# Kernel optimization log

Measured on AMD Instinct MI355X. Metric: run time of the kernel, lower is better.

Reference implementation:

```python
import jax, jax.numpy as jnp
import numpy as np

NUM_REL = 8
NUM_NODE = 100000
TYPED_NUM_NODE = 50000   # typed_num_node per relation (static)
EDGES_PER_REL = 800000   # avg degree 16
IN_C = 128
HID_C = 128


def setup_inputs() -> dict:
    key = jax.random.key(0)
    k1, k2, k3, k4, k5 = jax.random.split(key, 5)
    x = jax.random.normal(k1, (NUM_NODE, IN_C), dtype=jnp.float32)
    rel_weight = jax.random.normal(k2, (NUM_REL, IN_C, HID_C), dtype=jnp.float32) * 0.05
    sub_ptr = jnp.sort(jax.random.randint(k3, (NUM_REL, TYPED_NUM_NODE + 1), 0, EDGES_PER_REL), axis=-1)
    sub_idx = jax.random.randint(k4, (NUM_REL, EDGES_PER_REL), 0, NUM_NODE)
    sub_target = jax.random.randint(k5, (NUM_REL, TYPED_NUM_NODE), 0, NUM_NODE)
    return {"x": x, "rel_weight": rel_weight, "sub_ptr": sub_ptr,
            "sub_idx": sub_idx, "sub_target": sub_target}


def _csr_segment_ids(ptr):
    # CSR ptr [N+1] -> per-edge destination segment id [E]
    e = jnp.arange(EDGES_PER_REL)
    return jnp.clip(jnp.searchsorted(ptr, e, side='right') - 1, 0, TYPED_NUM_NODE - 1)


def reference(x, rel_weight, sub_ptr, sub_idx, sub_target):
    outs = []
    for r in range(NUM_REL):  # small fixed relation count
        seg = _csr_segment_ids(sub_ptr[r])
        # sage_sum_forward: sum neighbor features per destination node
        agg = jax.ops.segment_sum(x[sub_idx[r]], seg, num_segments=TYPED_NUM_NODE)  # [T, C]
        outs.append(agg @ rel_weight[r])  # [T, H]
    arr = jnp.concatenate(outs, axis=0)            # [R*T, H]
    tgt = sub_target.reshape(-1)                   # [R*T]
    out = jnp.zeros((NUM_NODE, HID_C), dtype=x.dtype).at[tgt].add(arr)
    return out
```

## Files before the change

kernel.cpp:

```cpp
#include <hip/hip_runtime.h>

#define NREL 8
#define NNODE 100000
#define TNODE 50000
#define NEDGE 800000
#define C 128
#define TILE_T 64
#define NTILE ((TNODE + TILE_T - 1) / TILE_T)
#define NENT (NREL * TNODE)
#define NB_SCAN ((NNODE + 255) / 256)

typedef unsigned int u32;
typedef unsigned short u16;
typedef __attribute__((ext_vector_type(8))) short bf16x8;
typedef __attribute__((ext_vector_type(4))) float f32x4;
typedef __attribute__((ext_vector_type(2))) float f32x2;

__device__ __forceinline__ u16 f2bf(float f) {
    union { float f; u32 u; } c; c.f = f;
    u32 u = c.u + 0x7FFFu + ((c.u >> 16) & 1u);
    return (u16)(u >> 16);
}
__device__ __forceinline__ u32 pack2(float a, float b) {
    return (u32)f2bf(a) | ((u32)f2bf(b) << 16);
}
__device__ __forceinline__ float2 unpack_bf2(u32 p) {
    union { u32 u; float f; } a, b;
    a.u = p << 16; b.u = p & 0xFFFF0000u;
    return make_float2(a.f, b.f);
}
__device__ __forceinline__ f32x2 bits2(u32 p) {
    union { u32 u[2]; f32x2 f; } c;
    c.u[0] = p << 16; c.u[1] = p & 0xFFFF0000u;
    return c.f;
}
__device__ __forceinline__ void addp(f32x2* a, uint4 v) {
    a[0] += bits2(v.x); a[1] += bits2(v.y);
    a[2] += bits2(v.z); a[3] += bits2(v.w);
}
__device__ __forceinline__ void fma4(float4& acc, float a, float w0, float w1, float w2, float w3) {
    acc.x = fmaf(a, w0, acc.x);
    acc.y = fmaf(a, w1, acc.y);
    acc.z = fmaf(a, w2, acc.z);
    acc.w = fmaf(a, w3, acc.w);
}

__global__ __launch_bounds__(256)
void convert_x_kernel(const float* __restrict__ x, u16* __restrict__ xb, int n4) {
    int i = blockIdx.x * 256 + threadIdx.x;
    const int stride = gridDim.x * 256;
    for (; i < n4; i += stride) {
        const float4 v = ((const float4*)x)[i];
        ushort4 o;
        o.x = f2bf(v.x); o.y = f2bf(v.y); o.z = f2bf(v.z); o.w = f2bf(v.w);
        ((ushort4*)xb)[i] = o;
    }
}

__global__ __launch_bounds__(256)
void convert_w_kernel(const float* __restrict__ w, u16* __restrict__ wtb) {
    const int o = blockIdx.x * 256 + threadIdx.x;
    if (o < NREL * C * C) {
        const int r = o >> 14, rem = o & 16383, cc = rem >> 7, k = rem & 127;
        wtb[o] = f2bf(w[(r << 14) + k * C + cc]);
    }
}

__global__ __launch_bounds__(256)
void hist_kernel(const int* __restrict__ tgt, int* __restrict__ count) {
    const int g = blockIdx.x * 256 + threadIdx.x;
    if (g < NENT) atomicAdd(&count[tgt[g]], 1);
}

__global__ __launch_bounds__(256)
void scan1_kernel(const int* __restrict__ count, int* __restrict__ bsum,
                  int* __restrict__ offsets, int* __restrict__ cursor) {
    __shared__ int s[256];
    const int tid = threadIdx.x;
    const int i = blockIdx.x * 256 + tid;
    const int v = (i < NNODE) ? count[i] : 0;
    s[tid] = v;
    __syncthreads();
    for (int st = 1; st < 256; st <<= 1) {
        const int t = (tid >= st) ? s[tid - st] : 0;
        __syncthreads();
        s[tid] += t;
        __syncthreads();
    }
    if (i < NNODE) {
        const int loc = s[tid] - v;
        offsets[i] = loc;
        cursor[i]  = loc;
    }
    if (tid == 255) bsum[blockIdx.x] = s[255];
}

__global__ __launch_bounds__(512)
void scan2_kernel(int* __restrict__ bsum) {
    __shared__ int s[512];
    const int tid = threadIdx.x;
    const int v = (tid < NB_SCAN) ? bsum[tid] : 0;
    s[tid] = v;
    __syncthreads();
    for (int st = 1; st < 512; st <<= 1) {
        const int t = (tid >= st) ? s[tid - st] : 0;
        __syncthreads();
        s[tid] += t;
        __syncthreads();
    }
    if (tid < NB_SCAN) bsum[tid] = s[tid] - v;
}

__global__ __launch_bounds__(256)
void fill_kernel(const int* __restrict__ tgt, int* __restrict__ cursor,
                 const int* __restrict__ bsum, int* __restrict__ list) {
    const int g = blockIdx.x * 256 + threadIdx.x;
    if (g < NENT) {
        const int t = tgt[g];
        const int pos = atomicAdd(&cursor[t], 1) + bsum[t >> 8];
        list[pos] = g;
    }
}

__global__ __launch_bounds__(512, 8)
void fused_gather_gemm_kernel(const u16* __restrict__ xb, const int* __restrict__ ptr,
                              const int* __restrict__ idx, const u16* __restrict__ wtb,
                              u16* __restrict__ P) {
    __shared__ u16 sA[TILE_T * 136];
    __shared__ int qcount;

    const int tid  = threadIdx.x;
    const int tile = blockIdx.x;
    const int r    = blockIdx.y;
    const int w    = tid >> 6;
    const int lane = tid & 63;

    if (tid == 0) qcount = 0;
    __syncthreads();

    const int* pr = ptr + r * (TNODE + 1);
    const int* er = idx + (size_t)r * NEDGE;
    const int q  = lane >> 4;
    const int sl = lane & 15;
    const u16* xcol = xb + sl * 8;

    for (;;) {
        int tl;
        if (lane == 0) tl = atomicAdd(&qcount, 1);
        tl = __shfl(tl, 0);
        if (tl >= TILE_T) break;

        const int t = tile * TILE_T + tl;
        f32x2 accA[4], accB[4];
        #pragma unroll
        for (int j = 0; j < 4; ++j) { accA[j] = (f32x2){0.f, 0.f}; accB[j] = (f32x2){0.f, 0.f}; }

        if (t < TNODE) {
            const int start = (t == 0) ? 0 : pr[t];
            const int end   = (t == TNODE - 1) ? NEDGE : pr[t + 1];

            for (int base = start; base < end; base += 64) {
                const int cnt = min(end - base, 64);
                int myi = (lane < cnt) ? er[base + lane] : 0;
                int i = 0;
                for (; i + 8 <= cnt; i += 8) {
                    const int sA0 = __shfl(myi, i + q);
                    const int sB0 = __shfl(myi, i + 4 + q);
                    const uint4 vA = *(const uint4*)(xcol + (size_t)sA0 * C);
                    const uint4 vB = *(const uint4*)(xcol + (size_t)sB0 * C);
                    addp(accA, vA);
                    addp(accB, vB);
                }
                if (i + 4 <= cnt) {
                    const int sA0 = __shfl(myi, i + q);
                    const uint4 vA = *(const uint4*)(xcol + (size_t)sA0 * C);
                    addp(accA, vA);
                    i += 4;
                }
                if (i < cnt) {
                    const int rem = cnt - i;
                    const int sA0 = __shfl(myi, i + ((q < rem) ? q : 0));
                    if (q < rem) {
                        const uint4 vA = *(const uint4*)(xcol + (size_t)sA0 * C);
                        addp(accA, vA);
                    }
                }
            }
        }
        #pragma unroll
        for (int j = 0; j < 4; ++j) {
            accA[j] += accB[j];
            accA[j].x += __shfl_xor(accA[j].x, 16);
            accA[j].y += __shfl_xor(accA[j].y, 16);
            accA[j].x += __shfl_xor(accA[j].x, 32);
            accA[j].y += __shfl_xor(accA[j].y, 32);
        }
        if (q == 0) {
            uint4 o;
            o.x = pack2(accA[0].x, accA[0].y);
            o.y = pack2(accA[1].x, accA[1].y);
            o.z = pack2(accA[2].x, accA[2].y);
            o.w = pack2(accA[3].x, accA[3].y);
            *(uint4*)(sA + tl * 136 + sl * 8) = o;
        }
    }
    __syncthreads();

    const int wr    = (w & 3) * 16;
    const int cbase = (w >> 2) * 4;
    const int fr    = lane & 15;
    const int fq    = lane >> 4;
    const u16* wb   = wtb + (size_t)r * C * C;

    f32x4 acc[4];
    #pragma unroll
    for (int cf = 0; cf < 4; ++cf) acc[cf] = (f32x4){0.f, 0.f, 0.f, 0.f};

    #pragma unroll
    for (int ks = 0; ks < 4; ++ks) {
        const bf16x8 a = *(const bf16x8*)(sA + (wr + fr) * 136 + ks * 32 + fq * 8);
        #pragma unroll
        for (int cf = 0; cf < 4; ++cf) {
            const bf16x8 b = *(const bf16x8*)(wb + ((cbase + cf) * 16 + fr) * C + ks * 32 + fq * 8);
            acc[cf] = __builtin_amdgcn_mfma_f32_16x16x32_bf16(a, b, acc[cf], 0, 0, 0);
        }
    }
    __syncthreads();

    #pragma unroll
    for (int cf = 0; cf < 4; ++cf) {
        #pragma unroll
        for (int j = 0; j < 4; ++j) {
            const int row = wr + fq * 4 + j;
            sA[row * 136 + (cbase + cf) * 16 + fr] = f2bf(acc[cf][j]);
        }
    }
    __syncthreads();

    #pragma unroll
    for (int i = 0; i < 2; ++i) {
        const int f = tid + i * 512;
        const int row = f >> 4, unit = f & 15;
        const int t = tile * TILE_T + row;
        if (t < TNODE)
            *(uint4*)(P + ((size_t)r * TNODE + t) * C + unit * 8) =
                *(const uint4*)(sA + row * 136 + unit * 8);
    }
}

__global__ __launch_bounds__(256)
void out_gather_kernel(const u16* __restrict__ P, const int* __restrict__ offsets,
                       const int* __restrict__ count, const int* __restrict__ bsum,
                       const int* __restrict__ list, float* __restrict__ out) {
    const int lane = threadIdx.x & 63;
    const int n = blockIdx.x * 4 + (threadIdx.x >> 6);
    if (n >= NNODE) return;
    const int st = offsets[n] + bsum[n >> 8];
    const int en = st + count[n];
    float2 a0 = make_float2(0.f, 0.f), a1 = make_float2(0.f, 0.f);
    int i = st;
    for (; i + 2 <= en; i += 2) {
        const u32 v0 = ((const u32*)(P + (size_t)list[i] * C))[lane];
        const u32 v1 = ((const u32*)(P + (size_t)list[i + 1] * C))[lane];
        const float2 f0 = unpack_bf2(v0), f1 = unpack_bf2(v1);
        a0.x += f0.x; a0.y += f0.y;
        a1.x += f1.x; a1.y += f1.y;
    }
    if (i < en) {
        const float2 f0 = unpack_bf2(((const u32*)(P + (size_t)list[i] * C))[lane]);
        a0.x += f0.x; a0.y += f0.y;
    }
    a0.x += a1.x; a0.y += a1.y;
    ((float2*)(out + (size_t)n * C))[lane] = a0;
}

__device__ __forceinline__ void add4(float4& acc, const float4& b) {
    acc.x += b.x; acc.y += b.y; acc.z += b.z; acc.w += b.w;
}
__global__ __launch_bounds__(256, 1)
void rgcn_fused_kernel(const float* __restrict__ x, const float* __restrict__ w,
                       const int* __restrict__ ptr, const int* __restrict__ idx,
                       const int* __restrict__ tgt, float* __restrict__ out) {
    __shared__ float sW[C * C];
    __shared__ float sAgg[TILE_T][C + 4];
    const int tid = threadIdx.x, tile = blockIdx.x, r = blockIdx.y;
    {
        const float4* src = (const float4*)(w + (size_t)r * C * C);
        float4* dst = (float4*)sW;
        #pragma unroll
        for (int i = 0; i < 16; ++i) dst[tid + i * 256] = src[tid + i * 256];
    }
    {
        const int tl = tid >> 2, g = tid & 3;
        const int t = tile * TILE_T + tl;
        float4 a[8];
        #pragma unroll
        for (int j = 0; j < 8; ++j) a[j] = make_float4(0.f, 0.f, 0.f, 0.f);
        if (t < TNODE) {
            const int* pr = ptr + (size_t)r * (TNODE + 1);
            const int* er = idx + (size_t)r * NEDGE;
            int e = (t == 0) ? 0 : pr[t];
            const int end = (t == TNODE - 1) ? NEDGE : pr[t + 1];
            for (; e < end; ++e) {
                const int s0 = er[e];
                const float4* r0 = (const float4*)(x + (size_t)s0 * C) + g * 8;
                #pragma unroll
                for (int j = 0; j < 8; ++j) add4(a[j], r0[j]);
            }
        }
        float* rowp = &sAgg[tl][g * 32];
        #pragma unroll
        for (int j = 0; j < 8; ++j) ((float4*)rowp)[j] = a[j];
    }
    __syncthreads();
    const int tg = tid >> 4, cg = tid & 15;
    float4 acc0[4], acc1[4];
    #pragma unroll
    for (int i = 0; i < 4; ++i) {
        acc0[i] = make_float4(0.f, 0.f, 0.f, 0.f);
        acc1[i] = make_float4(0.f, 0.f, 0.f, 0.f);
    }
    for (int k4 = 0; k4 < C / 4; ++k4) {
        float4 av[4];
        #pragma unroll
        for (int i = 0; i < 4; ++i) av[i] = *(const float4*)&sAgg[tg * 4 + i][k4 * 4];
        #pragma unroll
        for (int kk = 0; kk < 4; ++kk) {
            const int k = k4 * 4 + kk;
            const float4 w0 = *(const float4*)&sW[k * C + cg * 4];
            const float4 w1 = *(const float4*)&sW[k * C + 64 + cg * 4];
            #pragma unroll
            for (int i = 0; i < 4; ++i) {
                const float a = ((const float*)&av[i])[kk];
                fma4(acc0[i], a, w0.x, w0.y, w0.z, w0.w);
                fma4(acc1[i], a, w1.x, w1.y, w1.z, w1.w);
            }
        }
    }
    const int* tr = tgt + (size_t)r * TNODE;
    #pragma unroll
    for (int i = 0; i < 4; ++i) {
        const int t = tile * TILE_T + tg * 4 + i;
        if (t < TNODE) {
            const int node = tr[t];
            float* ob = out + (size_t)node * C + cg * 4;
            unsafeAtomicAdd(ob + 0, acc0[i].x);  unsafeAtomicAdd(ob + 1, acc0[i].y);
            unsafeAtomicAdd(ob + 2, acc0[i].z);  unsafeAtomicAdd(ob + 3, acc0[i].w);
            unsafeAtomicAdd(ob + 64, acc1[i].x); unsafeAtomicAdd(ob + 65, acc1[i].y);
            unsafeAtomicAdd(ob + 66, acc1[i].z); unsafeAtomicAdd(ob + 67, acc1[i].w);
        }
    }
}

extern "C" void kernel_launch(void* const* d_in, const int* in_sizes, int n_in,
                              void* d_out, int out_size, void* d_ws, size_t ws_size,
                              hipStream_t stream) {
    const float* x   = (const float*)d_in[0];
    const float* w   = (const float*)d_in[1];
    const int*   ptr = (const int*)d_in[2];
    const int*   idx = (const int*)d_in[3];
    const int*   tgt = (const int*)d_in[4];
    float* out = (float*)d_out;

    const size_t WS_NEED = 135000000;
    char* base = (char*)d_ws;

    if (ws_size >= WS_NEED) {
        u16* P       = (u16*)(base + 0);
        u16* xb      = (u16*)(base + 104000000);
        u16* wtb     = (u16*)(base + 130000000);
        int* count   = (int*)(base + 131000000);
        int* offsets = (int*)(base + 131500000);
        int* cursor  = (int*)(base + 132000000);
        int* bsum    = (int*)(base + 132500000);
        int* list    = (int*)(base + 133000000);

        convert_x_kernel<<<2048, 256, 0, stream>>>(x, xb, NNODE * C / 4);
        convert_w_kernel<<<(NREL * C * C + 255) / 256, 256, 0, stream>>>(w, wtb);

        hipMemsetAsync(count, 0, NNODE * sizeof(int), stream);
        hist_kernel<<<(NENT + 255) / 256, 256, 0, stream>>>(tgt, count);
        scan1_kernel<<<NB_SCAN, 256, 0, stream>>>(count, bsum, offsets, cursor);
        scan2_kernel<<<1, 512, 0, stream>>>(bsum);
        fill_kernel<<<(NENT + 255) / 256, 256, 0, stream>>>(tgt, cursor, bsum, list);

        dim3 grid(NTILE, NREL);
        fused_gather_gemm_kernel<<<grid, 512, 0, stream>>>(xb, ptr, idx, wtb, P);

        out_gather_kernel<<<(NNODE + 3) / 4, 256, 0, stream>>>(P, offsets, count, bsum, list, out);
    } else {
        hipMemsetAsync(out, 0, (size_t)NNODE * C * sizeof(float), stream);
        dim3 grid(NTILE, NREL);
        rgcn_fused_kernel<<<grid, 256, 0, stream>>>(x, w, ptr, idx, tgt, out);
    }
}
```

Measured before the change: 368.1 us.

## Fuse setup kernels and stage relation weights in LDS for MFMA

Combines the x conversion, weight transpose-conversion and count zeroing into a single launch, removing two kernel launches and a memset. In the fused gather-GEMM kernel, the per-relation bf16 weight matrix is first copied into a padded shared-memory buffer and the MFMA B operands are read from it instead of global memory. This adds about 34KB of LDS per block and lowers the occupancy hint from 8 to 6 blocks. Every tile now reloads the full 32KB weight matrix even though it reads each element once, so LDS pressure could cut occupancy during the gather phase.

```diff
diff --git a/kernel.cpp b/kernel.cpp
--- a/kernel.cpp
+++ b/kernel.cpp
@@ -10,6 +10,10 @@
 #define NENT (NREL * TNODE)
 #define NB_SCAN ((NNODE + 255) / 256)
 
+#define NB_CVX (NNODE * C / 4 / 256)
+#define NB_CVW (NREL * C * C / 256)
+#define NB_ZERO NB_SCAN
+
 typedef unsigned int u32;
 typedef unsigned short u16;
 typedef __attribute__((ext_vector_type(8))) short bf16x8;
@@ -46,23 +50,24 @@
 }
 
 __global__ __launch_bounds__(256)
-void convert_x_kernel(const float* __restrict__ x, u16* __restrict__ xb, int n4) {
-    int i = blockIdx.x * 256 + threadIdx.x;
-    const int stride = gridDim.x * 256;
-    for (; i < n4; i += stride) {
+void setup_kernel(const float* __restrict__ x, u16* __restrict__ xb,
+                  const float* __restrict__ w, u16* __restrict__ wtb,
+                  int* __restrict__ count) {
+    const int b = blockIdx.x;
+    const int tid = threadIdx.x;
+    if (b < NB_CVX) {
+        const int i = b * 256 + tid;
         const float4 v = ((const float4*)x)[i];
         ushort4 o;
         o.x = f2bf(v.x); o.y = f2bf(v.y); o.z = f2bf(v.z); o.w = f2bf(v.w);
         ((ushort4*)xb)[i] = o;
-    }
-}
-
-__global__ __launch_bounds__(256)
-void convert_w_kernel(const float* __restrict__ w, u16* __restrict__ wtb) {
-    const int o = blockIdx.x * 256 + threadIdx.x;
-    if (o < NREL * C * C) {
+    } else if (b < NB_CVX + NB_CVW) {
+        const int o = (b - NB_CVX) * 256 + tid;
         const int r = o >> 14, rem = o & 16383, cc = rem >> 7, k = rem & 127;
         wtb[o] = f2bf(w[(r << 14) + k * C + cc]);
+    } else {
+        const int i = (b - NB_CVX - NB_CVW) * 256 + tid;
+        if (i < NNODE) count[i] = 0;
     }
 }
 
@@ -122,10 +127,11 @@
     }
 }
 
-__global__ __launch_bounds__(512, 8)
+__global__ __launch_bounds__(512, 6)
 void fused_gather_gemm_kernel(const u16* __restrict__ xb, const int* __restrict__ ptr,
                               const int* __restrict__ idx, const u16* __restrict__ wtb,
                               u16* __restrict__ P) {
+    __shared__ u16 sB[C * 136];
     __shared__ u16 sA[TILE_T * 136];
     __shared__ int qcount;
 
@@ -135,6 +141,15 @@
     const int w    = tid >> 6;
     const int lane = tid & 63;
 
+    {
+        const uint4* src = (const uint4*)(wtb + (size_t)r * C * C);
+        #pragma unroll
+        for (int i = 0; i < 4; ++i) {
+            const int f = tid + i * 512;
+            const int col = f >> 4, unit = f & 15;
+            *(uint4*)(sB + col * 136 + unit * 8) = src[f];
+        }
+    }
     if (tid == 0) qcount = 0;
     __syncthreads();
 
@@ -210,7 +225,6 @@
     const int cbase = (w >> 2) * 4;
     const int fr    = lane & 15;
     const int fq    = lane >> 4;
-    const u16* wb   = wtb + (size_t)r * C * C;
 
     f32x4 acc[4];
     #pragma unroll
@@ -221,7 +235,7 @@
         const bf16x8 a = *(const bf16x8*)(sA + (wr + fr) * 136 + ks * 32 + fq * 8);
         #pragma unroll
         for (int cf = 0; cf < 4; ++cf) {
-            const bf16x8 b = *(const bf16x8*)(wb + ((cbase + cf) * 16 + fr) * C + ks * 32 + fq * 8);
+            const bf16x8 b = *(const bf16x8*)(sB + ((cbase + cf) * 16 + fr) * 136 + ks * 32 + fq * 8);
             acc[cf] = __builtin_amdgcn_mfma_f32_16x16x32_bf16(a, b, acc[cf], 0, 0, 0);
         }
     }
@@ -375,10 +389,7 @@
         int* bsum    = (int*)(base + 132500000);
         int* list    = (int*)(base + 133000000);
 
-        convert_x_kernel<<<2048, 256, 0, stream>>>(x, xb, NNODE * C / 4);
-        convert_w_kernel<<<(NREL * C * C + 255) / 256, 256, 0, stream>>>(w, wtb);
-
-        hipMemsetAsync(count, 0, NNODE * sizeof(int), stream);
+        setup_kernel<<<NB_CVX + NB_CVW + NB_ZERO, 256, 0, stream>>>(x, xb, w, wtb, count);
         hist_kernel<<<(NENT + 255) / 256, 256, 0, stream>>>(tgt, count);
         scan1_kernel<<<NB_SCAN, 256, 0, stream>>>(count, bsum, offsets, cursor);
         scan2_kernel<<<1, 512, 0, stream>>>(bsum);
```

Measured after the change: 339.9 us. 1.08x faster.
